# Kernel optimization log

Hardware: AMD Instinct MI355X
Metric: run time of the kernel (lower is better)

Reference implementation:

```python
import jax, jax.numpy as jnp
import numpy as np

N_NODES = 100000


def gcn_conv(x, W, b, src, dst, n):
    # PyG GCNConv with add_self_loops=True, symmetric normalization:
    # out = D^{-1/2} (A + I) D^{-1/2} X W + b
    loop = jnp.arange(n, dtype=src.dtype)
    src_f = jnp.concatenate([src, loop])
    dst_f = jnp.concatenate([dst, loop])
    deg = jax.ops.segment_sum(jnp.ones_like(src_f, dtype=x.dtype), dst_f, num_segments=n)
    dinv = jnp.where(deg > 0, jax.lax.rsqrt(deg), 0.0)
    norm = dinv[src_f] * dinv[dst_f]          # [E+N]
    h = x @ W                                  # [N, out]
    msg = h[src_f] * norm[:, None]             # gather + scale
    out = jax.ops.segment_sum(msg, dst_f, num_segments=n)  # scatter-add
    return out + b


def setup_inputs() -> dict:
    key = jax.random.key(0)
    k = jax.random.split(key, 8)
    x = jax.random.normal(k[0], (N_NODES, 128), dtype=jnp.float32)
    edge_index = jax.random.randint(k[1], (2, 1600000), 0, N_NODES, dtype=jnp.int64)
    s1 = 1.0 / np.sqrt(128)
    s2 = 1.0 / np.sqrt(64)
    s3 = 1.0 / np.sqrt(32)
    W1 = jax.random.uniform(k[2], (128, 64), jnp.float32, -s1, s1)
    b1 = jnp.zeros((64,), jnp.float32)
    W2 = jax.random.uniform(k[3], (64, 32), jnp.float32, -s2, s2)
    b2 = jnp.zeros((32,), jnp.float32)
    Wfc = jax.random.uniform(k[4], (32, 1), jnp.float32, -s3, s3)
    bfc = jax.random.uniform(k[5], (1,), jnp.float32, -s3, s3)
    return {"x": x, "edge_index": edge_index, "W1": W1, "b1": b1,
            "W2": W2, "b2": b2, "Wfc": Wfc, "bfc": bfc}


def reference(x, edge_index, W1, b1, W2, b2, Wfc, bfc):
    n = x.shape[0]
    src, dst = edge_index[0], edge_index[1]
    h = jax.nn.relu(gcn_conv(x, W1, b1, src, dst, n))
    h = jax.nn.relu(gcn_conv(h, W2, b2, src, dst, n))
    out = h @ Wfc + bfc                        # [N, 1]
    return out.reshape(-1)
```

## Files before the change

kernel.cpp:

```cpp
#include <hip/hip_runtime.h>
#include <hip/hip_bf16.h>
#include <stdint.h>


#define THREADS 256
#define NBUCK_MAX 1024
#define CAP 4096
#define CAPB_LOG 12
#define SC_EPT 16

typedef __attribute__((ext_vector_type(8))) short short8;
typedef __attribute__((ext_vector_type(4))) float f32x4;
union frag_u { uint4 u4; short8 s8; };

__device__ __forceinline__ unsigned int pack_bf2(float a, float b) {
    unsigned int ua = __float_as_uint(a);
    unsigned int ub = __float_as_uint(b);
    ua = (ua + 0x7FFFu + ((ua >> 16) & 1u)) >> 16;
    ub = (ub + 0x7FFFu + ((ub >> 16) & 1u)) >> 16;
    return ua | (ub << 16);
}
__device__ __forceinline__ unsigned short bf16r(float a) {
    unsigned int ua = __float_as_uint(a);
    return (unsigned short)((ua + 0x7FFFu + ((ua >> 16) & 1u)) >> 16);
}
__device__ __forceinline__ float bf_lo(unsigned int u) { return __uint_as_float(u << 16); }
__device__ __forceinline__ float bf_hi(unsigned int u) { return __uint_as_float(u & 0xFFFF0000u); }

__device__ __forceinline__ int detect64(const unsigned int* w) {
    int is64 = 1;
    #pragma unroll
    for (int i = 1; i < 64; i += 2) {
        if (w[i] != 0u) { is64 = 0; break; }
    }
    return is64;
}

__global__ void k_prep(int* bucket_cursor, int B,
                       const float* __restrict__ W1, const float* __restrict__ W2,
                       uint4* __restrict__ w1f, uint4* __restrict__ w2f) {
    int b = blockIdx.x;
    int t = threadIdx.x;
    if (b == 0) {
        for (int i = t; i < 1024; i += THREADS) {
            int l = i & 63;
            int f = i >> 6;
            int ct = f >> 2, kt = f & 3;
            int c = ct * 16 + (l & 15);
            int k0 = kt * 32 + (l >> 4) * 8;
            unsigned int r0 = pack_bf2(W1[(k0 + 0) * 64 + c], W1[(k0 + 1) * 64 + c]);
            unsigned int r1 = pack_bf2(W1[(k0 + 2) * 64 + c], W1[(k0 + 3) * 64 + c]);
            unsigned int r2 = pack_bf2(W1[(k0 + 4) * 64 + c], W1[(k0 + 5) * 64 + c]);
            unsigned int r3 = pack_bf2(W1[(k0 + 6) * 64 + c], W1[(k0 + 7) * 64 + c]);
            w1f[i] = make_uint4(r0, r1, r2, r3);
        }
        {
            int l = t & 63;
            int f = t >> 6;
            int ct = f >> 1, kt = f & 1;
            int c = ct * 16 + (l & 15);
            int k0 = kt * 32 + (l >> 4) * 8;
            unsigned int r0 = pack_bf2(W2[(k0 + 0) * 32 + c], W2[(k0 + 1) * 32 + c]);
            unsigned int r1 = pack_bf2(W2[(k0 + 2) * 32 + c], W2[(k0 + 3) * 32 + c]);
            unsigned int r2 = pack_bf2(W2[(k0 + 4) * 32 + c], W2[(k0 + 5) * 32 + c]);
            unsigned int r3 = pack_bf2(W2[(k0 + 6) * 32 + c], W2[(k0 + 7) * 32 + c]);
            w2f[t] = make_uint4(r0, r1, r2, r3);
        }
    } else {
        int i = (b - 1) * THREADS + t;
        if (i < B) bucket_cursor[i] = i << CAPB_LOG;
    }
}

__global__ void k_bucket_scatter(const void* ei, int* bucket_cursor,
                                 unsigned int* packed, int E, int B) {
    __shared__ int h[NBUCK_MAX];
    __shared__ int base[NBUCK_MAX];
    __shared__ int is64s;
    int t = threadIdx.x;
    if (t == 0) is64s = detect64((const unsigned int*)ei);
    for (int i = t; i < B; i += THREADS) h[i] = 0;
    __syncthreads();
    bool is64 = (is64s != 0);
    int lo = blockIdx.x * (THREADS * SC_EPT);
    const long long* p64 = (const long long*)ei;
    const int* p32 = (const int*)ei;

    int srcv[SC_EPT], dstv[SC_EPT];
    if (is64) {
        #pragma unroll
        for (int i = 0; i < SC_EPT; ++i) {
            int e = lo + i * THREADS + t;
            int ec = (e < E) ? e : (E - 1);
            srcv[i] = (int)p64[ec];
            dstv[i] = (e < E) ? (int)p64[(size_t)E + ec] : -1;
        }
    } else {
        #pragma unroll
        for (int i = 0; i < SC_EPT; ++i) {
            int e = lo + i * THREADS + t;
            int ec = (e < E) ? e : (E - 1);
            srcv[i] = p32[ec];
            dstv[i] = (e < E) ? p32[E + ec] : -1;
        }
    }
    #pragma unroll
    for (int i = 0; i < SC_EPT; ++i)
        if (dstv[i] >= 0) atomicAdd(&h[dstv[i] >> 7], 1);
    __syncthreads();
    for (int i = t; i < B; i += THREADS) {
        int c = h[i];
        base[i] = c ? atomicAdd(&bucket_cursor[i], c) : 0;
    }
    __syncthreads();
    for (int i = t; i < B; i += THREADS) h[i] = 0;
    __syncthreads();
    #pragma unroll
    for (int i = 0; i < SC_EPT; ++i) {
        if (dstv[i] >= 0) {
            int b = dstv[i] >> 7;
            int pos = base[b] + atomicAdd(&h[b], 1);
            packed[pos] = (unsigned int)srcv[i] | ((unsigned int)(dstv[i] & 127) << 25);
        }
    }
}

__global__ void k_fine_sort(const unsigned int* __restrict__ packed,
                            const int* __restrict__ bucket_cursor,
                            int* __restrict__ csr, int* __restrict__ offsets,
                            int* __restrict__ countp, float* __restrict__ dinv,
                            int n, int B) {
    __shared__ unsigned int words[CAP];
    __shared__ int srcstage[CAP];
    __shared__ int cnt[128];
    __shared__ int scanv[128];
    __shared__ int cursor[128];
    int b = blockIdx.x;
    int t = threadIdx.x;
    int base = b << CAPB_LOG;
    int size = bucket_cursor[b] - base;
    if (t < 128) cnt[t] = 0;
    __syncthreads();
    for (int i0 = 0; i0 < size; i0 += THREADS) {
        int i = i0 + t;
        if (i < size) {
            unsigned int w = packed[base + i];
            words[i] = w;
            atomicAdd(&cnt[(w >> 25) & 127], 1);
        }
    }
    __syncthreads();
    if (t < 128) scanv[t] = cnt[t];
    __syncthreads();
    for (int off = 1; off < 128; off <<= 1) {
        int v = 0;
        if (t < 128 && t >= off) v = scanv[t - off];
        __syncthreads();
        if (t < 128) scanv[t] += v;
        __syncthreads();
    }
    if (t < 128) {
        int ex = scanv[t] - cnt[t];
        scanv[t] = ex;
        cursor[t] = ex;
        int node = (b << 7) + t;
        if (node < n) {
            offsets[node] = base + ex;
            countp[node] = cnt[t];
            dinv[node] = rsqrtf((float)(cnt[t] + 1));
        }
    }
    __syncthreads();
    for (int i0 = 0; i0 < size; i0 += THREADS) {
        int i = i0 + t;
        if (i < size) {
            unsigned int w = words[i];
            int d = (w >> 25) & 127;
            int rank = atomicAdd(&cursor[d], 1);
            srcstage[rank] = (int)(w & 0x1FFFFFFu);
        }
    }
    __syncthreads();
    for (int i0 = 0; i0 < size; i0 += THREADS) {
        int i = i0 + t;
        if (i < size) csr[base + i] = srcstage[i];
    }
}

__global__ void __launch_bounds__(THREADS) k_gemm1(const float* __restrict__ x,
                                                   const uint4* __restrict__ w1f,
                                                   const float* __restrict__ dinv,
                                                   unsigned short* __restrict__ hs1, int n) {
    int t = threadIdx.x;
    int w = t >> 6, l = t & 63;
    int rowbase = blockIdx.x * 64 + w * 16;

    uint4 bfr[16];
    #pragma unroll
    for (int f = 0; f < 16; ++f) bfr[f] = w1f[f * 64 + l];

    f32x4 acc[4];
    #pragma unroll
    for (int ct = 0; ct < 4; ++ct) acc[ct] = (f32x4){0.f, 0.f, 0.f, 0.f};

    int arow = rowbase + (l & 15);
    bool rv = (arow < n);
    const float* xp = x + (size_t)arow * 128 + (l >> 4) * 8;

    #pragma unroll
    for (int kt = 0; kt < 4; ++kt) {
        float4 a0 = make_float4(0.f, 0.f, 0.f, 0.f), a1 = a0;
        if (rv) {
            a0 = ((const float4*)(xp + kt * 32))[0];
            a1 = ((const float4*)(xp + kt * 32))[1];
        }
        frag_u af;
        af.u4 = make_uint4(pack_bf2(a0.x, a0.y), pack_bf2(a0.z, a0.w),
                           pack_bf2(a1.x, a1.y), pack_bf2(a1.z, a1.w));
        #pragma unroll
        for (int ct = 0; ct < 4; ++ct) {
            frag_u bfu; bfu.u4 = bfr[ct * 4 + kt];
            acc[ct] = __builtin_amdgcn_mfma_f32_16x16x32_bf16(af.s8, bfu.s8, acc[ct], 0, 0, 0);
        }
    }

    int orow0 = rowbase + (l >> 4) * 4;
    #pragma unroll
    for (int reg = 0; reg < 4; ++reg) {
        int r = orow0 + reg;
        if (r < n) {
            float dv = dinv[r];
            #pragma unroll
            for (int ct = 0; ct < 4; ++ct)
                hs1[(size_t)r * 64 + ct * 16 + (l & 15)] = bf16r(acc[ct][reg] * dv);
        }
    }
}

__global__ void k_agg1(const unsigned int* __restrict__ hs1, const int* __restrict__ csr,
                       const int* __restrict__ offsets, const int* __restrict__ count,
                       const float* __restrict__ dinv, const float* __restrict__ b1,
                       unsigned int* __restrict__ h1post, int n) {
    int wid = threadIdx.x >> 6;
    int lane = threadIdx.x & 63;
    int node = blockIdx.x * 4 + wid;
    if (node >= n) return;
    int g  = lane >> 4;
    int f4 = lane & 15;
    int s = offsets[node];
    int c = count[node];
    const uint2* tab = (const uint2*)hs1;

    float4 a0 = make_float4(0.f, 0.f, 0.f, 0.f);
    float4 a1 = a0, a2 = a0, a3 = a0;
    if (g == 0) {
        uint2 sv = tab[(size_t)node * 16 + f4];
        a0 = make_float4(bf_lo(sv.x), bf_hi(sv.x), bf_lo(sv.y), bf_hi(sv.y));
    }

    for (int j0 = 0; j0 < c; j0 += 64) {
        int cc = min(c - j0, 64);
        int idx = csr[s + j0 + min(lane, cc - 1)];
        for (int j = 0; j < cc; j += 16) {
            int e0 = j + g, e1 = e0 + 4, e2 = e0 + 8, e3 = e0 + 12;
            int s0 = __shfl(idx, min(e0, cc - 1));
            int s1 = __shfl(idx, min(e1, cc - 1));
            int s2 = __shfl(idx, min(e2, cc - 1));
            int s3 = __shfl(idx, min(e3, cc - 1));
            uint2 u0 = tab[(size_t)s0 * 16 + f4];
            uint2 u1 = tab[(size_t)s1 * 16 + f4];
            uint2 u2 = tab[(size_t)s2 * 16 + f4];
            uint2 u3 = tab[(size_t)s3 * 16 + f4];
            float m0 = (e0 < cc) ? 1.f : 0.f;
            float m1 = (e1 < cc) ? 1.f : 0.f;
            float m2 = (e2 < cc) ? 1.f : 0.f;
            float m3 = (e3 < cc) ? 1.f : 0.f;
            a0.x = fmaf(m0, bf_lo(u0.x), a0.x); a0.y = fmaf(m0, bf_hi(u0.x), a0.y);
            a0.z = fmaf(m0, bf_lo(u0.y), a0.z); a0.w = fmaf(m0, bf_hi(u0.y), a0.w);
            a1.x = fmaf(m1, bf_lo(u1.x), a1.x); a1.y = fmaf(m1, bf_hi(u1.x), a1.y);
            a1.z = fmaf(m1, bf_lo(u1.y), a1.z); a1.w = fmaf(m1, bf_hi(u1.y), a1.w);
            a2.x = fmaf(m2, bf_lo(u2.x), a2.x); a2.y = fmaf(m2, bf_hi(u2.x), a2.y);
            a2.z = fmaf(m2, bf_lo(u2.y), a2.z); a2.w = fmaf(m2, bf_hi(u2.y), a2.w);
            a3.x = fmaf(m3, bf_lo(u3.x), a3.x); a3.y = fmaf(m3, bf_hi(u3.x), a3.y);
            a3.z = fmaf(m3, bf_lo(u3.y), a3.z); a3.w = fmaf(m3, bf_hi(u3.y), a3.w);
        }
    }
    a0.x += a1.x + a2.x + a3.x;
    a0.y += a1.y + a2.y + a3.y;
    a0.z += a1.z + a2.z + a3.z;
    a0.w += a1.w + a2.w + a3.w;
    a0.x += __shfl_xor(a0.x, 16); a0.y += __shfl_xor(a0.y, 16);
    a0.z += __shfl_xor(a0.z, 16); a0.w += __shfl_xor(a0.w, 16);
    a0.x += __shfl_xor(a0.x, 32); a0.y += __shfl_xor(a0.y, 32);
    a0.z += __shfl_xor(a0.z, 32); a0.w += __shfl_xor(a0.w, 32);

    if (g == 0) {
        float dv = dinv[node];
        float4 b = ((const float4*)b1)[f4];
        float ox = fmaxf(fmaf(dv, a0.x, b.x), 0.f);
        float oy = fmaxf(fmaf(dv, a0.y, b.y), 0.f);
        float oz = fmaxf(fmaf(dv, a0.z, b.z), 0.f);
        float ow = fmaxf(fmaf(dv, a0.w, b.w), 0.f);
        uint2 o;
        o.x = pack_bf2(ox, oy);
        o.y = pack_bf2(oz, ow);
        ((uint2*)h1post)[(size_t)node * 16 + f4] = o;
    }
}

__global__ void __launch_bounds__(THREADS) k_gemm2(const uint4* __restrict__ h1,
                                                   const uint4* __restrict__ w2f,
                                                   const float* __restrict__ dinv,
                                                   unsigned short* __restrict__ hs2, int n) {
    int t = threadIdx.x;
    int w = t >> 6, l = t & 63;
    int rowbase = blockIdx.x * 64 + w * 16;

    uint4 bfr[4];
    #pragma unroll
    for (int f = 0; f < 4; ++f) bfr[f] = w2f[f * 64 + l];

    f32x4 acc[2];
    acc[0] = (f32x4){0.f, 0.f, 0.f, 0.f};
    acc[1] = (f32x4){0.f, 0.f, 0.f, 0.f};

    int arow = rowbase + (l & 15);
    bool rv = (arow < n);
    const uint4* hp = h1 + (size_t)arow * 8 + (l >> 4);

    #pragma unroll
    for (int kt = 0; kt < 2; ++kt) {
        frag_u af;
        af.u4 = rv ? hp[kt * 4] : make_uint4(0u, 0u, 0u, 0u);
        #pragma unroll
        for (int ct = 0; ct < 2; ++ct) {
            frag_u bfu; bfu.u4 = bfr[ct * 2 + kt];
            acc[ct] = __builtin_amdgcn_mfma_f32_16x16x32_bf16(af.s8, bfu.s8, acc[ct], 0, 0, 0);
        }
    }

    int orow0 = rowbase + (l >> 4) * 4;
    #pragma unroll
    for (int reg = 0; reg < 4; ++reg) {
        int r = orow0 + reg;
        if (r < n) {
            float dv = dinv[r];
            #pragma unroll
            for (int ct = 0; ct < 2; ++ct)
                hs2[(size_t)r * 32 + ct * 16 + (l & 15)] = bf16r(acc[ct][reg] * dv);
        }
    }
}

__global__ void k_agg2_head(const unsigned int* __restrict__ hs2, const int* __restrict__ csr,
                            const int* __restrict__ offsets, const int* __restrict__ count,
                            const float* __restrict__ dinv, const float* __restrict__ b2,
                            const float* __restrict__ Wfc, const float* __restrict__ bfc,
                            float* __restrict__ out, int n) {
    int wid = threadIdx.x >> 6;
    int lane = threadIdx.x & 63;
    int node = blockIdx.x * 4 + wid;
    if (node >= n) return;
    int g  = lane >> 3;
    int f4 = lane & 7;
    int s = offsets[node];
    int c = count[node];
    const uint2* tab = (const uint2*)hs2;

    float4 a0 = make_float4(0.f, 0.f, 0.f, 0.f);
    float4 a1 = a0;
    if (g == 0) {
        uint2 sv = tab[(size_t)node * 8 + f4];
        a0 = make_float4(bf_lo(sv.x), bf_hi(sv.x), bf_lo(sv.y), bf_hi(sv.y));
    }

    for (int j0 = 0; j0 < c; j0 += 64) {
        int cc = min(c - j0, 64);
        int idx = csr[s + j0 + min(lane, cc - 1)];
        for (int j = 0; j < cc; j += 16) {
            int e0 = j + g, e1 = e0 + 8;
            int s0 = __shfl(idx, min(e0, cc - 1));
            int s1 = __shfl(idx, min(e1, cc - 1));
            uint2 u0 = tab[(size_t)s0 * 8 + f4];
            uint2 u1 = tab[(size_t)s1 * 8 + f4];
            float m0 = (e0 < cc) ? 1.f : 0.f;
            float m1 = (e1 < cc) ? 1.f : 0.f;
            a0.x = fmaf(m0, bf_lo(u0.x), a0.x); a0.y = fmaf(m0, bf_hi(u0.x), a0.y);
            a0.z = fmaf(m0, bf_lo(u0.y), a0.z); a0.w = fmaf(m0, bf_hi(u0.y), a0.w);
            a1.x = fmaf(m1, bf_lo(u1.x), a1.x); a1.y = fmaf(m1, bf_hi(u1.x), a1.y);
            a1.z = fmaf(m1, bf_lo(u1.y), a1.z); a1.w = fmaf(m1, bf_hi(u1.y), a1.w);
        }
    }
    a0.x += a1.x; a0.y += a1.y; a0.z += a1.z; a0.w += a1.w;
    #pragma unroll
    for (int m = 8; m <= 32; m <<= 1) {
        a0.x += __shfl_xor(a0.x, m); a0.y += __shfl_xor(a0.y, m);
        a0.z += __shfl_xor(a0.z, m); a0.w += __shfl_xor(a0.w, m);
    }

    float dv = dinv[node];
    float4 b = ((const float4*)b2)[f4];
    float4 w = ((const float4*)Wfc)[f4];
    float hx = fmaxf(fmaf(dv, a0.x, b.x), 0.f);
    float hy = fmaxf(fmaf(dv, a0.y, b.y), 0.f);
    float hz = fmaxf(fmaf(dv, a0.z, b.z), 0.f);
    float hw = fmaxf(fmaf(dv, a0.w, b.w), 0.f);
    float p = hx * w.x + hy * w.y + hz * w.z + hw * w.w;
    p += __shfl_xor(p, 1);
    p += __shfl_xor(p, 2);
    p += __shfl_xor(p, 4);
    if (lane == 0) out[node] = p + bfc[0];
}

extern "C" void kernel_launch(void* const* d_in, const int* in_sizes, int n_in,
                              void* d_out, int out_size, void* d_ws, size_t ws_size,
                              hipStream_t stream) {
    const float* x   = (const float*)d_in[0];
    const void*  ei  = d_in[1];
    const float* W1  = (const float*)d_in[2];
    const float* b1  = (const float*)d_in[3];
    const float* W2  = (const float*)d_in[4];
    const float* b2  = (const float*)d_in[5];
    const float* Wfc = (const float*)d_in[6];
    const float* bfc = (const float*)d_in[7];
    float* out = (float*)d_out;

    const int n = in_sizes[0] / 128;
    const int E = in_sizes[1] / 2;
    const int B = (n + 127) >> 7;
    const size_t BCAP = (size_t)B << CAPB_LOG;

    size_t off = 0;
    auto alloc = [&](size_t bytes) -> void* {
        void* p = (char*)d_ws + off;
        off += (bytes + 255) & ~(size_t)255;
        return p;
    };
    int*   bucket_cursor = (int*)alloc((size_t)NBUCK_MAX * 4);
    unsigned int* packed = (unsigned int*)alloc(BCAP * 4);
    int*   csr     = (int*)  alloc(BCAP * 4);
    int*   offsets = (int*)  alloc((size_t)n * 4);
    int*   count   = (int*)  alloc((size_t)n * 4);
    float* dinv    = (float*)alloc((size_t)n * 4);
    unsigned int* hs1    = (unsigned int*)alloc((size_t)n * 64 * 2);
    unsigned int* h1post = (unsigned int*)alloc((size_t)n * 64 * 2);
    unsigned int* hs2    = (unsigned int*)alloc((size_t)n * 32 * 2);
    uint4* w1f   = (uint4*)alloc(1024 * 16);
    uint4* w2f   = (uint4*)alloc(256 * 16);
    (void)ws_size;

    const int GB = (n + 63) / 64;
    const int AG = (n + 3) / 4;
    const int PREP = 1 + (B + THREADS - 1) / THREADS;
    const int SB = (E + THREADS * SC_EPT - 1) / (THREADS * SC_EPT);

    k_prep<<<PREP, THREADS, 0, stream>>>(bucket_cursor, B, W1, W2, w1f, w2f);
    k_bucket_scatter<<<SB, THREADS, 0, stream>>>(ei, bucket_cursor, packed, E, B);
    k_fine_sort<<<B, THREADS, 0, stream>>>(packed, bucket_cursor, csr, offsets, count, dinv, n, B);
    k_gemm1<<<GB, THREADS, 0, stream>>>(x, w1f, dinv, (unsigned short*)hs1, n);
    k_agg1<<<AG, THREADS, 0, stream>>>(hs1, csr, offsets, count, dinv, b1, h1post, n);
    k_gemm2<<<GB, THREADS, 0, stream>>>((const uint4*)h1post, w2f, dinv, (unsigned short*)hs2, n);
    k_agg2_head<<<AG, THREADS, 0, stream>>>(hs2, csr, offsets, count, dinv, b2, Wfc, bfc, out, n);
}
```

Baseline: 134.4 us.

## Fuse layer-2 GEMM into layer-1 aggregation and hoist int64 detection

Removes the separate gemm2 kernel and the h1post intermediate buffer. The layer-1 aggregation kernel now stages its ReLU output row in shared memory and multiplies it by W2, held in shared memory as fp32 with scalar FMAs, then writes the dinv-scaled bf16 hs2 directly. The int64 index-format detection moves to the prep kernel and is passed to the scatter kernel through a global flag, so every scatter block no longer repeats it. This saves one launch and a global write plus read of the 64-wide hidden features, but each block now loads W2 into shared memory and adds a block-wide barrier.

```diff
diff --git a/kernel.cpp b/kernel.cpp
--- a/kernel.cpp
+++ b/kernel.cpp
@@ -36,12 +36,13 @@
     return is64;
 }
 
-__global__ void k_prep(int* bucket_cursor, int B,
-                       const float* __restrict__ W1, const float* __restrict__ W2,
-                       uint4* __restrict__ w1f, uint4* __restrict__ w2f) {
+__global__ void k_prep(const unsigned int* ei_words, int* flag,
+                       int* bucket_cursor, int B,
+                       const float* __restrict__ W1, uint4* __restrict__ w1f) {
     int b = blockIdx.x;
     int t = threadIdx.x;
     if (b == 0) {
+        if (t == 0) *flag = detect64(ei_words);
         for (int i = t; i < 1024; i += THREADS) {
             int l = i & 63;
             int f = i >> 6;
@@ -54,34 +55,20 @@
             unsigned int r3 = pack_bf2(W1[(k0 + 6) * 64 + c], W1[(k0 + 7) * 64 + c]);
             w1f[i] = make_uint4(r0, r1, r2, r3);
         }
-        {
-            int l = t & 63;
-            int f = t >> 6;
-            int ct = f >> 1, kt = f & 1;
-            int c = ct * 16 + (l & 15);
-            int k0 = kt * 32 + (l >> 4) * 8;
-            unsigned int r0 = pack_bf2(W2[(k0 + 0) * 32 + c], W2[(k0 + 1) * 32 + c]);
-            unsigned int r1 = pack_bf2(W2[(k0 + 2) * 32 + c], W2[(k0 + 3) * 32 + c]);
-            unsigned int r2 = pack_bf2(W2[(k0 + 4) * 32 + c], W2[(k0 + 5) * 32 + c]);
-            unsigned int r3 = pack_bf2(W2[(k0 + 6) * 32 + c], W2[(k0 + 7) * 32 + c]);
-            w2f[t] = make_uint4(r0, r1, r2, r3);
-        }
     } else {
         int i = (b - 1) * THREADS + t;
         if (i < B) bucket_cursor[i] = i << CAPB_LOG;
     }
 }
 
-__global__ void k_bucket_scatter(const void* ei, int* bucket_cursor,
-                                 unsigned int* packed, int E, int B) {
+__global__ void k_bucket_scatter(const void* ei, const int* __restrict__ flag,
+                                 int* bucket_cursor, unsigned int* packed, int E, int B) {
     __shared__ int h[NBUCK_MAX];
     __shared__ int base[NBUCK_MAX];
-    __shared__ int is64s;
     int t = threadIdx.x;
-    if (t == 0) is64s = detect64((const unsigned int*)ei);
     for (int i = t; i < B; i += THREADS) h[i] = 0;
-    __syncthreads();
-    bool is64 = (is64s != 0);
+    bool is64 = (*flag != 0);
+    __syncthreads();
     int lo = blockIdx.x * (THREADS * SC_EPT);
     const long long* p64 = (const long long*)ei;
     const int* p32 = (const int*)ei;
@@ -237,118 +224,95 @@
     }
 }
 
-__global__ void k_agg1(const unsigned int* __restrict__ hs1, const int* __restrict__ csr,
-                       const int* __restrict__ offsets, const int* __restrict__ count,
-                       const float* __restrict__ dinv, const float* __restrict__ b1,
-                       unsigned int* __restrict__ h1post, int n) {
-    int wid = threadIdx.x >> 6;
-    int lane = threadIdx.x & 63;
+__global__ void k_agg1_fused(const unsigned int* __restrict__ hs1, const int* __restrict__ csr,
+                             const int* __restrict__ offsets, const int* __restrict__ count,
+                             const float* __restrict__ dinv, const float* __restrict__ b1,
+                             const float* __restrict__ W2,
+                             unsigned int* __restrict__ hs2, int n) {
+    __shared__ float W2s[64 * 32];
+    __shared__ float h1row[4][64];
+    int t = threadIdx.x;
+    #pragma unroll
+    for (int i = 0; i < 2; ++i)
+        ((float4*)W2s)[t + i * THREADS] = ((const float4*)W2)[t + i * THREADS];
+
+    int wid = t >> 6;
+    int lane = t & 63;
     int node = blockIdx.x * 4 + wid;
-    if (node >= n) return;
+    bool valid = (node < n);
     int g  = lane >> 4;
     int f4 = lane & 15;
-    int s = offsets[node];
-    int c = count[node];
     const uint2* tab = (const uint2*)hs1;
 
-    float4 a0 = make_float4(0.f, 0.f, 0.f, 0.f);
-    float4 a1 = a0, a2 = a0, a3 = a0;
-    if (g == 0) {
-        uint2 sv = tab[(size_t)node * 16 + f4];
-        a0 = make_float4(bf_lo(sv.x), bf_hi(sv.x), bf_lo(sv.y), bf_hi(sv.y));
-    }
-
-    for (int j0 = 0; j0 < c; j0 += 64) {
-        int cc = min(c - j0, 64);
-        int idx = csr[s + j0 + min(lane, cc - 1)];
-        for (int j = 0; j < cc; j += 16) {
-            int e0 = j + g, e1 = e0 + 4, e2 = e0 + 8, e3 = e0 + 12;
-            int s0 = __shfl(idx, min(e0, cc - 1));
-            int s1 = __shfl(idx, min(e1, cc - 1));
-            int s2 = __shfl(idx, min(e2, cc - 1));
-            int s3 = __shfl(idx, min(e3, cc - 1));
-            uint2 u0 = tab[(size_t)s0 * 16 + f4];
-            uint2 u1 = tab[(size_t)s1 * 16 + f4];
-            uint2 u2 = tab[(size_t)s2 * 16 + f4];
-            uint2 u3 = tab[(size_t)s3 * 16 + f4];
-            float m0 = (e0 < cc) ? 1.f : 0.f;
-            float m1 = (e1 < cc) ? 1.f : 0.f;
-            float m2 = (e2 < cc) ? 1.f : 0.f;
-            float m3 = (e3 < cc) ? 1.f : 0.f;
-            a0.x = fmaf(m0, bf_lo(u0.x), a0.x); a0.y = fmaf(m0, bf_hi(u0.x), a0.y);
-            a0.z = fmaf(m0, bf_lo(u0.y), a0.z); a0.w = fmaf(m0, bf_hi(u0.y), a0.w);
-            a1.x = fmaf(m1, bf_lo(u1.x), a1.x); a1.y = fmaf(m1, bf_hi(u1.x), a1.y);
-            a1.z = fmaf(m1, bf_lo(u1.y), a1.z); a1.w = fmaf(m1, bf_hi(u1.y), a1.w);
-            a2.x = fmaf(m2, bf_lo(u2.x), a2.x); a2.y = fmaf(m2, bf_hi(u2.x), a2.y);
-            a2.z = fmaf(m2, bf_lo(u2.y), a2.z); a2.w = fmaf(m2, bf_hi(u2.y), a2.w);
-            a3.x = fmaf(m3, bf_lo(u3.x), a3.x); a3.y = fmaf(m3, bf_hi(u3.x), a3.y);
-            a3.z = fmaf(m3, bf_lo(u3.y), a3.z); a3.w = fmaf(m3, bf_hi(u3.y), a3.w);
-        }
-    }
-    a0.x += a1.x + a2.x + a3.x;
-    a0.y += a1.y + a2.y + a3.y;
-    a0.z += a1.z + a2.z + a3.z;
-    a0.w += a1.w + a2.w + a3.w;
-    a0.x += __shfl_xor(a0.x, 16); a0.y += __shfl_xor(a0.y, 16);
-    a0.z += __shfl_xor(a0.z, 16); a0.w += __shfl_xor(a0.w, 16);
-    a0.x += __shfl_xor(a0.x, 32); a0.y += __shfl_xor(a0.y, 32);
-    a0.z += __shfl_xor(a0.z, 32); a0.w += __shfl_xor(a0.w, 32);
-
-    if (g == 0) {
-        float dv = dinv[node];
-        float4 b = ((const float4*)b1)[f4];
-        float ox = fmaxf(fmaf(dv, a0.x, b.x), 0.f);
-        float oy = fmaxf(fmaf(dv, a0.y, b.y), 0.f);
-        float oz = fmaxf(fmaf(dv, a0.z, b.z), 0.f);
-        float ow = fmaxf(fmaf(dv, a0.w, b.w), 0.f);
-        uint2 o;
-        o.x = pack_bf2(ox, oy);
-        o.y = pack_bf2(oz, ow);
-        ((uint2*)h1post)[(size_t)node * 16 + f4] = o;
-    }
-}
-
-__global__ void __launch_bounds__(THREADS) k_gemm2(const uint4* __restrict__ h1,
-                                                   const uint4* __restrict__ w2f,
-                                                   const float* __restrict__ dinv,
-                                                   unsigned short* __restrict__ hs2, int n) {
-    int t = threadIdx.x;
-    int w = t >> 6, l = t & 63;
-    int rowbase = blockIdx.x * 64 + w * 16;
-
-    uint4 bfr[4];
-    #pragma unroll
-    for (int f = 0; f < 4; ++f) bfr[f] = w2f[f * 64 + l];
-
-    f32x4 acc[2];
-    acc[0] = (f32x4){0.f, 0.f, 0.f, 0.f};
-    acc[1] = (f32x4){0.f, 0.f, 0.f, 0.f};
-
-    int arow = rowbase + (l & 15);
-    bool rv = (arow < n);
-    const uint4* hp = h1 + (size_t)arow * 8 + (l >> 4);
-
-    #pragma unroll
-    for (int kt = 0; kt < 2; ++kt) {
-        frag_u af;
-        af.u4 = rv ? hp[kt * 4] : make_uint4(0u, 0u, 0u, 0u);
+    if (valid) {
+        int s = offsets[node];
+        int c = count[node];
+        float4 a0 = make_float4(0.f, 0.f, 0.f, 0.f);
+        float4 a1 = a0, a2 = a0, a3 = a0;
+        if (g == 0) {
+            uint2 sv = tab[(size_t)node * 16 + f4];
+            a0 = make_float4(bf_lo(sv.x), bf_hi(sv.x), bf_lo(sv.y), bf_hi(sv.y));
+        }
+        for (int j0 = 0; j0 < c; j0 += 64) {
+            int cc = min(c - j0, 64);
+            int idx = csr[s + j0 + min(lane, cc - 1)];
+            for (int j = 0; j < cc; j += 16) {
+                int e0 = j + g, e1 = e0 + 4, e2 = e0 + 8, e3 = e0 + 12;
+                int s0 = __shfl(idx, min(e0, cc - 1));
+                int s1 = __shfl(idx, min(e1, cc - 1));
+                int s2 = __shfl(idx, min(e2, cc - 1));
+                int s3 = __shfl(idx, min(e3, cc - 1));
+                uint2 u0 = tab[(size_t)s0 * 16 + f4];
+                uint2 u1 = tab[(size_t)s1 * 16 + f4];
+                uint2 u2 = tab[(size_t)s2 * 16 + f4];
+                uint2 u3 = tab[(size_t)s3 * 16 + f4];
+                float m0 = (e0 < cc) ? 1.f : 0.f;
+                float m1 = (e1 < cc) ? 1.f : 0.f;
+                float m2 = (e2 < cc) ? 1.f : 0.f;
+                float m3 = (e3 < cc) ? 1.f : 0.f;
+                a0.x = fmaf(m0, bf_lo(u0.x), a0.x); a0.y = fmaf(m0, bf_hi(u0.x), a0.y);
+                a0.z = fmaf(m0, bf_lo(u0.y), a0.z); a0.w = fmaf(m0, bf_hi(u0.y), a0.w);
+                a1.x = fmaf(m1, bf_lo(u1.x), a1.x); a1.y = fmaf(m1, bf_hi(u1.x), a1.y);
+                a1.z = fmaf(m1, bf_lo(u1.y), a1.z); a1.w = fmaf(m1, bf_hi(u1.y), a1.w);
+                a2.x = fmaf(m2, bf_lo(u2.x), a2.x); a2.y = fmaf(m2, bf_hi(u2.x), a2.y);
+                a2.z = fmaf(m2, bf_lo(u2.y), a2.z); a2.w = fmaf(m2, bf_hi(u2.y), a2.w);
+                a3.x = fmaf(m3, bf_lo(u3.x), a3.x); a3.y = fmaf(m3, bf_hi(u3.x), a3.y);
+                a3.z = fmaf(m3, bf_lo(u3.y), a3.z); a3.w = fmaf(m3, bf_hi(u3.y), a3.w);
+            }
+        }
+        a0.x += a1.x + a2.x + a3.x;
+        a0.y += a1.y + a2.y + a3.y;
+        a0.z += a1.z + a2.z + a3.z;
+        a0.w += a1.w + a2.w + a3.w;
+        a0.x += __shfl_xor(a0.x, 16); a0.y += __shfl_xor(a0.y, 16);
+        a0.z += __shfl_xor(a0.z, 16); a0.w += __shfl_xor(a0.w, 16);
+        a0.x += __shfl_xor(a0.x, 32); a0.y += __shfl_xor(a0.y, 32);
+        a0.z += __shfl_xor(a0.z, 32); a0.w += __shfl_xor(a0.w, 32);
+
+        if (g == 0) {
+            float dv = dinv[node];
+            float4 b = ((const float4*)b1)[f4];
+            float ox = fmaxf(fmaf(dv, a0.x, b.x), 0.f);
+            float oy = fmaxf(fmaf(dv, a0.y, b.y), 0.f);
+            float oz = fmaxf(fmaf(dv, a0.z, b.z), 0.f);
+            float ow = fmaxf(fmaf(dv, a0.w, b.w), 0.f);
+            ((float4*)h1row[wid])[f4] = make_float4(ox, oy, oz, ow);
+        }
+    }
+    __syncthreads();
+    if (valid) {
+        int col = lane & 31, half = lane >> 5;
+        const float* hr = h1row[wid] + half * 32;
+        const float* wp = W2s + half * 32 * 32 + col;
+        float p = 0.f;
         #pragma unroll
-        for (int ct = 0; ct < 2; ++ct) {
-            frag_u bfu; bfu.u4 = bfr[ct * 2 + kt];
-            acc[ct] = __builtin_amdgcn_mfma_f32_16x16x32_bf16(af.s8, bfu.s8, acc[ct], 0, 0, 0);
-        }
-    }
-
-    int orow0 = rowbase + (l >> 4) * 4;
-    #pragma unroll
-    for (int reg = 0; reg < 4; ++reg) {
-        int r = orow0 + reg;
-        if (r < n) {
-            float dv = dinv[r];
-            #pragma unroll
-            for (int ct = 0; ct < 2; ++ct)
-                hs2[(size_t)r * 32 + ct * 16 + (l & 15)] = bf16r(acc[ct][reg] * dv);
-        }
+        for (int k = 0; k < 32; ++k)
+            p = fmaf(hr[k], wp[k * 32], p);
+        p += __shfl_xor(p, 32);
+        p *= dinv[node];
+        float q = __shfl_xor(p, 1);
+        if (half == 0 && (lane & 1) == 0)
+            hs2[(size_t)node * 16 + (lane >> 1)] = pack_bf2(p, q);
     }
 }
 
@@ -442,11 +406,10 @@
     int*   offsets = (int*)  alloc((size_t)n * 4);
     int*   count   = (int*)  alloc((size_t)n * 4);
     float* dinv    = (float*)alloc((size_t)n * 4);
-    unsigned int* hs1    = (unsigned int*)alloc((size_t)n * 64 * 2);
-    unsigned int* h1post = (unsigned int*)alloc((size_t)n * 64 * 2);
-    unsigned int* hs2    = (unsigned int*)alloc((size_t)n * 32 * 2);
+    unsigned int* hs1 = (unsigned int*)alloc((size_t)n * 64 * 2);
+    unsigned int* hs2 = (unsigned int*)alloc((size_t)n * 32 * 2);
     uint4* w1f   = (uint4*)alloc(1024 * 16);
-    uint4* w2f   = (uint4*)alloc(256 * 16);
+    int*   flag  = (int*)  alloc(4);
     (void)ws_size;
 
     const int GB = (n + 63) / 64;
@@ -454,11 +417,10 @@
     const int PREP = 1 + (B + THREADS - 1) / THREADS;
     const int SB = (E + THREADS * SC_EPT - 1) / (THREADS * SC_EPT);
 
-    k_prep<<<PREP, THREADS, 0, stream>>>(bucket_cursor, B, W1, W2, w1f, w2f);
-    k_bucket_scatter<<<SB, THREADS, 0, stream>>>(ei, bucket_cursor, packed, E, B);
+    k_prep<<<PREP, THREADS, 0, stream>>>((const unsigned int*)ei, flag, bucket_cursor, B, W1, w1f);
+    k_bucket_scatter<<<SB, THREADS, 0, stream>>>(ei, flag, bucket_cursor, packed, E, B);
     k_fine_sort<<<B, THREADS, 0, stream>>>(packed, bucket_cursor, csr, offsets, count, dinv, n, B);
     k_gemm1<<<GB, THREADS, 0, stream>>>(x, w1f, dinv, (unsigned short*)hs1, n);
-    k_agg1<<<AG, THREADS, 0, stream>>>(hs1, csr, offsets, count, dinv, b1, h1post, n);
-    k_gemm2<<<GB, THREADS, 0, stream>>>((const uint4*)h1post, w2f, dinv, (unsigned short*)hs2, n);
+    k_agg1_fused<<<AG, THREADS, 0, stream>>>(hs1, csr, offsets, count, dinv, b1, W2, hs2, n);
     k_agg2_head<<<AG, THREADS, 0, stream>>>(hs2, csr, offsets, count, dinv, b2, Wfc, bfc, out, n);
 }
```

Result: slower. 141.6 us (+5.4%).

## Fuse edge bucket scatter with layer-1 GEMM and move source dinv scaling into aggregation

Applied to the files above, without the earlier changes.

The layer-1 GEMM no longer depends on dinv, so its blocks now run in the same launch as the edge bucket scatter, overlapping compute-bound MFMA work with the atomic-heavy scatter. The source-side dinv scaling moves into k_agg1, which gathers dinv[src] per edge. The 64/32-bit detection moves into k_prep and is passed through a flag. This removes one launch and lets the two phases share the GPU, at the cost of an extra random dinv gather per edge in aggregation and one more bf16 rounding point.

```diff
diff --git a/kernel.cpp b/kernel.cpp
--- a/kernel.cpp
+++ b/kernel.cpp
@@ -36,12 +36,14 @@
     return is64;
 }
 
-__global__ void k_prep(int* bucket_cursor, int B,
+__global__ void k_prep(const unsigned int* ei_words, int* flag,
+                       int* bucket_cursor, int B,
                        const float* __restrict__ W1, const float* __restrict__ W2,
                        uint4* __restrict__ w1f, uint4* __restrict__ w2f) {
     int b = blockIdx.x;
     int t = threadIdx.x;
     if (b == 0) {
+        if (t == 0) *flag = detect64(ei_words);
         for (int i = t; i < 1024; i += THREADS) {
             int l = i & 63;
             int f = i >> 6;
@@ -72,55 +74,103 @@
     }
 }
 
-__global__ void k_bucket_scatter(const void* ei, int* bucket_cursor,
-                                 unsigned int* packed, int E, int B) {
+__global__ void __launch_bounds__(THREADS) k_scatter_gemm1(
+        const void* ei, const int* __restrict__ flag,
+        int* bucket_cursor, unsigned int* packed, int E, int B, int SB,
+        const float* __restrict__ x, const uint4* __restrict__ w1f,
+        unsigned short* __restrict__ hs1, int n) {
     __shared__ int h[NBUCK_MAX];
     __shared__ int base[NBUCK_MAX];
-    __shared__ int is64s;
     int t = threadIdx.x;
-    if (t == 0) is64s = detect64((const unsigned int*)ei);
-    for (int i = t; i < B; i += THREADS) h[i] = 0;
-    __syncthreads();
-    bool is64 = (is64s != 0);
-    int lo = blockIdx.x * (THREADS * SC_EPT);
-    const long long* p64 = (const long long*)ei;
-    const int* p32 = (const int*)ei;
-
-    int srcv[SC_EPT], dstv[SC_EPT];
-    if (is64) {
+
+    if ((int)blockIdx.x < SB) {
+        for (int i = t; i < B; i += THREADS) h[i] = 0;
+        bool is64 = (*flag != 0);
+        __syncthreads();
+        int lo = blockIdx.x * (THREADS * SC_EPT);
+        const long long* p64 = (const long long*)ei;
+        const int* p32 = (const int*)ei;
+
+        int srcv[SC_EPT], dstv[SC_EPT];
+        if (is64) {
+            #pragma unroll
+            for (int i = 0; i < SC_EPT; ++i) {
+                int e = lo + i * THREADS + t;
+                int ec = (e < E) ? e : (E - 1);
+                srcv[i] = (int)p64[ec];
+                dstv[i] = (e < E) ? (int)p64[(size_t)E + ec] : -1;
+            }
+        } else {
+            #pragma unroll
+            for (int i = 0; i < SC_EPT; ++i) {
+                int e = lo + i * THREADS + t;
+                int ec = (e < E) ? e : (E - 1);
+                srcv[i] = p32[ec];
+                dstv[i] = (e < E) ? p32[E + ec] : -1;
+            }
+        }
+        #pragma unroll
+        for (int i = 0; i < SC_EPT; ++i)
+            if (dstv[i] >= 0) atomicAdd(&h[dstv[i] >> 7], 1);
+        __syncthreads();
+        for (int i = t; i < B; i += THREADS) {
+            int c = h[i];
+            base[i] = c ? atomicAdd(&bucket_cursor[i], c) : 0;
+        }
+        __syncthreads();
+        for (int i = t; i < B; i += THREADS) h[i] = 0;
+        __syncthreads();
         #pragma unroll
         for (int i = 0; i < SC_EPT; ++i) {
-            int e = lo + i * THREADS + t;
-            int ec = (e < E) ? e : (E - 1);
-            srcv[i] = (int)p64[ec];
-            dstv[i] = (e < E) ? (int)p64[(size_t)E + ec] : -1;
+            if (dstv[i] >= 0) {
+                int b = dstv[i] >> 7;
+                int pos = base[b] + atomicAdd(&h[b], 1);
+                packed[pos] = (unsigned int)srcv[i] | ((unsigned int)(dstv[i] & 127) << 25);
+            }
         }
     } else {
-        #pragma unroll
-        for (int i = 0; i < SC_EPT; ++i) {
-            int e = lo + i * THREADS + t;
-            int ec = (e < E) ? e : (E - 1);
-            srcv[i] = p32[ec];
-            dstv[i] = (e < E) ? p32[E + ec] : -1;
-        }
-    }
-    #pragma unroll
-    for (int i = 0; i < SC_EPT; ++i)
-        if (dstv[i] >= 0) atomicAdd(&h[dstv[i] >> 7], 1);
-    __syncthreads();
-    for (int i = t; i < B; i += THREADS) {
-        int c = h[i];
-        base[i] = c ? atomicAdd(&bucket_cursor[i], c) : 0;
-    }
-    __syncthreads();
-    for (int i = t; i < B; i += THREADS) h[i] = 0;
-    __syncthreads();
-    #pragma unroll
-    for (int i = 0; i < SC_EPT; ++i) {
-        if (dstv[i] >= 0) {
-            int b = dstv[i] >> 7;
-            int pos = base[b] + atomicAdd(&h[b], 1);
-            packed[pos] = (unsigned int)srcv[i] | ((unsigned int)(dstv[i] & 127) << 25);
+        int gb = blockIdx.x - SB;
+        int w = t >> 6, l = t & 63;
+        int rowbase = gb * 64 + w * 16;
+
+        uint4 bfr[16];
+        #pragma unroll
+        for (int f = 0; f < 16; ++f) bfr[f] = w1f[f * 64 + l];
+
+        f32x4 acc[4];
+        #pragma unroll
+        for (int ct = 0; ct < 4; ++ct) acc[ct] = (f32x4){0.f, 0.f, 0.f, 0.f};
+
+        int arow = rowbase + (l & 15);
+        bool rv = (arow < n);
+        const float* xp = x + (size_t)arow * 128 + (l >> 4) * 8;
+
+        #pragma unroll
+        for (int kt = 0; kt < 4; ++kt) {
+            float4 a0 = make_float4(0.f, 0.f, 0.f, 0.f), a1 = a0;
+            if (rv) {
+                a0 = ((const float4*)(xp + kt * 32))[0];
+                a1 = ((const float4*)(xp + kt * 32))[1];
+            }
+            frag_u af;
+            af.u4 = make_uint4(pack_bf2(a0.x, a0.y), pack_bf2(a0.z, a0.w),
+                               pack_bf2(a1.x, a1.y), pack_bf2(a1.z, a1.w));
+            #pragma unroll
+            for (int ct = 0; ct < 4; ++ct) {
+                frag_u bfu; bfu.u4 = bfr[ct * 4 + kt];
+                acc[ct] = __builtin_amdgcn_mfma_f32_16x16x32_bf16(af.s8, bfu.s8, acc[ct], 0, 0, 0);
+            }
+        }
+
+        int orow0 = rowbase + (l >> 4) * 4;
+        #pragma unroll
+        for (int reg = 0; reg < 4; ++reg) {
+            int r = orow0 + reg;
+            if (r < n) {
+                #pragma unroll
+                for (int ct = 0; ct < 4; ++ct)
+                    hs1[(size_t)r * 64 + ct * 16 + (l & 15)] = bf16r(acc[ct][reg]);
+            }
         }
     }
 }
@@ -187,56 +237,6 @@
     }
 }
 
-__global__ void __launch_bounds__(THREADS) k_gemm1(const float* __restrict__ x,
-                                                   const uint4* __restrict__ w1f,
-                                                   const float* __restrict__ dinv,
-                                                   unsigned short* __restrict__ hs1, int n) {
-    int t = threadIdx.x;
-    int w = t >> 6, l = t & 63;
-    int rowbase = blockIdx.x * 64 + w * 16;
-
-    uint4 bfr[16];
-    #pragma unroll
-    for (int f = 0; f < 16; ++f) bfr[f] = w1f[f * 64 + l];
-
-    f32x4 acc[4];
-    #pragma unroll
-    for (int ct = 0; ct < 4; ++ct) acc[ct] = (f32x4){0.f, 0.f, 0.f, 0.f};
-
-    int arow = rowbase + (l & 15);
-    bool rv = (arow < n);
-    const float* xp = x + (size_t)arow * 128 + (l >> 4) * 8;
-
-    #pragma unroll
-    for (int kt = 0; kt < 4; ++kt) {
-        float4 a0 = make_float4(0.f, 0.f, 0.f, 0.f), a1 = a0;
-        if (rv) {
-            a0 = ((const float4*)(xp + kt * 32))[0];
-            a1 = ((const float4*)(xp + kt * 32))[1];
-        }
-        frag_u af;
-        af.u4 = make_uint4(pack_bf2(a0.x, a0.y), pack_bf2(a0.z, a0.w),
-                           pack_bf2(a1.x, a1.y), pack_bf2(a1.z, a1.w));
-        #pragma unroll
-        for (int ct = 0; ct < 4; ++ct) {
-            frag_u bfu; bfu.u4 = bfr[ct * 4 + kt];
-            acc[ct] = __builtin_amdgcn_mfma_f32_16x16x32_bf16(af.s8, bfu.s8, acc[ct], 0, 0, 0);
-        }
-    }
-
-    int orow0 = rowbase + (l >> 4) * 4;
-    #pragma unroll
-    for (int reg = 0; reg < 4; ++reg) {
-        int r = orow0 + reg;
-        if (r < n) {
-            float dv = dinv[r];
-            #pragma unroll
-            for (int ct = 0; ct < 4; ++ct)
-                hs1[(size_t)r * 64 + ct * 16 + (l & 15)] = bf16r(acc[ct][reg] * dv);
-        }
-    }
-}
-
 __global__ void k_agg1(const unsigned int* __restrict__ hs1, const int* __restrict__ csr,
                        const int* __restrict__ offsets, const int* __restrict__ count,
                        const float* __restrict__ dinv, const float* __restrict__ b1,
@@ -249,13 +249,15 @@
     int f4 = lane & 15;
     int s = offsets[node];
     int c = count[node];
+    float dvn = dinv[node];
     const uint2* tab = (const uint2*)hs1;
 
     float4 a0 = make_float4(0.f, 0.f, 0.f, 0.f);
     float4 a1 = a0, a2 = a0, a3 = a0;
     if (g == 0) {
         uint2 sv = tab[(size_t)node * 16 + f4];
-        a0 = make_float4(bf_lo(sv.x), bf_hi(sv.x), bf_lo(sv.y), bf_hi(sv.y));
+        a0 = make_float4(dvn * bf_lo(sv.x), dvn * bf_hi(sv.x),
+                         dvn * bf_lo(sv.y), dvn * bf_hi(sv.y));
     }
 
     for (int j0 = 0; j0 < c; j0 += 64) {
@@ -267,14 +269,14 @@
             int s1 = __shfl(idx, min(e1, cc - 1));
             int s2 = __shfl(idx, min(e2, cc - 1));
             int s3 = __shfl(idx, min(e3, cc - 1));
+            float m0 = (e0 < cc) ? dinv[s0] : 0.f;
+            float m1 = (e1 < cc) ? dinv[s1] : 0.f;
+            float m2 = (e2 < cc) ? dinv[s2] : 0.f;
+            float m3 = (e3 < cc) ? dinv[s3] : 0.f;
             uint2 u0 = tab[(size_t)s0 * 16 + f4];
             uint2 u1 = tab[(size_t)s1 * 16 + f4];
             uint2 u2 = tab[(size_t)s2 * 16 + f4];
             uint2 u3 = tab[(size_t)s3 * 16 + f4];
-            float m0 = (e0 < cc) ? 1.f : 0.f;
-            float m1 = (e1 < cc) ? 1.f : 0.f;
-            float m2 = (e2 < cc) ? 1.f : 0.f;
-            float m3 = (e3 < cc) ? 1.f : 0.f;
             a0.x = fmaf(m0, bf_lo(u0.x), a0.x); a0.y = fmaf(m0, bf_hi(u0.x), a0.y);
             a0.z = fmaf(m0, bf_lo(u0.y), a0.z); a0.w = fmaf(m0, bf_hi(u0.y), a0.w);
             a1.x = fmaf(m1, bf_lo(u1.x), a1.x); a1.y = fmaf(m1, bf_hi(u1.x), a1.y);
@@ -295,12 +297,11 @@
     a0.z += __shfl_xor(a0.z, 32); a0.w += __shfl_xor(a0.w, 32);
 
     if (g == 0) {
-        float dv = dinv[node];
         float4 b = ((const float4*)b1)[f4];
-        float ox = fmaxf(fmaf(dv, a0.x, b.x), 0.f);
-        float oy = fmaxf(fmaf(dv, a0.y, b.y), 0.f);
-        float oz = fmaxf(fmaf(dv, a0.z, b.z), 0.f);
-        float ow = fmaxf(fmaf(dv, a0.w, b.w), 0.f);
+        float ox = fmaxf(fmaf(dvn, a0.x, b.x), 0.f);
+        float oy = fmaxf(fmaf(dvn, a0.y, b.y), 0.f);
+        float oz = fmaxf(fmaf(dvn, a0.z, b.z), 0.f);
+        float ow = fmaxf(fmaf(dvn, a0.w, b.w), 0.f);
         uint2 o;
         o.x = pack_bf2(ox, oy);
         o.y = pack_bf2(oz, ow);
@@ -447,6 +448,7 @@
     unsigned int* hs2    = (unsigned int*)alloc((size_t)n * 32 * 2);
     uint4* w1f   = (uint4*)alloc(1024 * 16);
     uint4* w2f   = (uint4*)alloc(256 * 16);
+    int*   flag  = (int*)  alloc(4);
     (void)ws_size;
 
     const int GB = (n + 63) / 64;
@@ -454,10 +456,11 @@
     const int PREP = 1 + (B + THREADS - 1) / THREADS;
     const int SB = (E + THREADS * SC_EPT - 1) / (THREADS * SC_EPT);
 
-    k_prep<<<PREP, THREADS, 0, stream>>>(bucket_cursor, B, W1, W2, w1f, w2f);
-    k_bucket_scatter<<<SB, THREADS, 0, stream>>>(ei, bucket_cursor, packed, E, B);
+    k_prep<<<PREP, THREADS, 0, stream>>>((const unsigned int*)ei, flag, bucket_cursor, B,
+                                         W1, W2, w1f, w2f);
+    k_scatter_gemm1<<<SB + GB, THREADS, 0, stream>>>(ei, flag, bucket_cursor, packed, E, B, SB,
+                                                     x, w1f, (unsigned short*)hs1, n);
     k_fine_sort<<<B, THREADS, 0, stream>>>(packed, bucket_cursor, csr, offsets, count, dinv, n, B);
-    k_gemm1<<<GB, THREADS, 0, stream>>>(x, w1f, dinv, (unsigned short*)hs1, n);
     k_agg1<<<AG, THREADS, 0, stream>>>(hs1, csr, offsets, count, dinv, b1, h1post, n);
     k_gemm2<<<GB, THREADS, 0, stream>>>((const uint4*)h1post, w2f, dinv, (unsigned short*)hs2, n);
     k_agg2_head<<<AG, THREADS, 0, stream>>>(hs2, csr, offsets, count, dinv, b2, Wfc, bfc, out, n);
```

Result: no change. 132.0 us, median of 2 (-1.7%).
